# Kernel optimization log

Measured on AMD Instinct MI355X. Metric: run time of the kernel, lower is better.

## Reference

```python
import jax, jax.numpy as jnp
import numpy as np

LN_EPS = 1e-5


def _layer_norm(x, g, b):
    mu = x.mean(-1, keepdims=True)
    var = ((x - mu) ** 2).mean(-1, keepdims=True)
    return (x - mu) / jnp.sqrt(var + LN_EPS) * g + b


def _process_memory(mem, mem_W, mem_b, ln_g, ln_b):
    # deep memory MLP: Linear -> LayerNorm -> SiLU per layer (dropout = identity in eval)
    h = mem
    for i in range(mem_W.shape[0]):
        h = jax.nn.silu(_layer_norm(h @ mem_W[i] + mem_b[i], ln_g[i], ln_b[i]))
    return h


def setup_inputs() -> dict:
    key = jax.random.key(0)
    B, S, D, M, L = 32, 2048, 1024, 1024, 2
    ks = jax.random.split(key, 12)
    s = 0.02
    inp = {
        'inputs': jax.random.normal(ks[0], (B, S, D), dtype=jnp.float32),
        'memory_state': jnp.zeros((B, M), dtype=jnp.float32),
        'momentum_state': jnp.zeros((B, M), dtype=jnp.float32),
        # projections (stored [in, out], equivalent to torch Linear weight.T)
        'Wk': jax.random.normal(ks[1], (D, M)) * s, 'bk': jnp.zeros((M,)),
        'Wv': jax.random.normal(ks[2], (D, M)) * s, 'bv': jnp.zeros((M,)),
        # deep memory layers, stacked over num_layers
        'mem_W': jax.random.normal(ks[3], (L, M, M)) * s,
        'mem_b': jnp.zeros((L, M)),
        'ln_g': jnp.ones((L, M)),
        'ln_b': jnp.zeros((L, M)),
        # gates: in = D + M
        'Wf': jax.random.normal(ks[4], (D + M, M)) * s, 'bf': jnp.zeros((M,)),
        'Wm': jax.random.normal(ks[5], (D + M, M)) * s, 'bm': jnp.zeros((M,)),
        'Wu': jax.random.normal(ks[6], (D + M, M)) * s, 'bu': jnp.zeros((M,)),
        'eta': jnp.ones((1,)) * 0.9,
        'theta': jnp.ones((1,)) * 0.1,
    }
    return inp


def reference(inputs, memory_state, momentum_state, Wk, bk, Wv, bv,
              mem_W, mem_b, ln_g, ln_b, Wf, bf, Wm, bm, Wu, bu, eta, theta):
    keys = inputs @ Wk + bk      # [B,S,M]
    values = inputs @ Wv + bv    # [B,S,M]

    def assoc_loss(mem):
        mo = _process_memory(mem, mem_W, mem_b, ln_g, ln_b)      # [B,M]
        pred = jnp.einsum('bsm,bm->bs', keys, mo)                # bmm(keys, mo^T)
        diff = pred[..., None] - values                          # expand to [B,S,M]
        return 0.5 * jnp.mean(diff ** 2)

    surprise_grad = jax.grad(assoc_loss)(memory_state)           # [B,M]

    pooled = inputs.mean(axis=1)                                 # [B,D]
    gate_in = jnp.concatenate([pooled, memory_state], axis=-1)   # [B,D+M]
    forget_g = jax.nn.sigmoid(gate_in @ Wf + bf)
    update_g = jax.nn.sigmoid(gate_in @ Wu + bu)
    # momentum_gate computed in source but unused in the update
    _ = jax.nn.sigmoid(gate_in @ Wm + bm)

    new_momentum = eta * momentum_state + theta * surprise_grad
    new_memory = (1.0 - forget_g) * memory_state + update_g * new_momentum

    processed = _process_memory(new_memory, mem_W, mem_b, ln_g, ln_b)
    return processed, jax.lax.stop_gradient(new_memory)
```

## Files before the change

### kernel.cpp

```cpp
#include <hip/hip_runtime.h>
#include <math.h>

#define Bc 32
#define Sc 2048
#define Dc 1024
#define Mc 1024
#define LNEPS 1e-5f
#define SCv (1.f/67108864.f)

__device__ __forceinline__ float4 f4add(float4 a, float4 b) {
    return make_float4(a.x + b.x, a.y + b.y, a.z + b.z, a.w + b.w);
}

__device__ __forceinline__ void dreduce(float& a, float& b, float* sm) {
#pragma unroll
    for (int o = 32; o; o >>= 1) { a += __shfl_xor(a, o); b += __shfl_xor(b, o); }
    int w = threadIdx.x >> 6;
    if ((threadIdx.x & 63) == 0) { sm[w] = a; sm[4 + w] = b; }
    __syncthreads();
    a = sm[0] + sm[1] + sm[2] + sm[3];
    b = sm[4] + sm[5] + sm[6] + sm[7];
    __syncthreads();
}

__device__ __forceinline__ void wreduce(float& a, float& b) {
#pragma unroll
    for (int o = 32; o; o >>= 1) { a += __shfl_xor(a, o); b += __shfl_xor(b, o); }
}

__device__ __forceinline__ void nt_map(int t, int& n0i, int& b0i, int& ks) {
    int xcd = t & 7, rest = t >> 3;
    b0i = rest & 3;
    int q = rest >> 2;
    int s = q * 8 + xcd;
    ks = s >> 4; n0i = s & 15;
}
__device__ __forceinline__ void t_map(int t, int& dc, int& b, int& mc) {
    int xcd = t & 7, rest = t >> 3;
    b = rest & 31;
    int q = rest >> 5;
    int s = q * 8 + xcd;
    dc = s >> 3; mc = s & 7;
}

__device__ __forceinline__ void load_A128(float* Atile, const float* A, int b0, int k0) {
    for (int i = threadIdx.x; i < 1024; i += 256) {
        int r = i >> 7, c = i & 127;
        Atile[i] = A[(size_t)(b0 + r) * 1024 + k0 + c];
    }
}

__device__ __forceinline__ void nt_inner128v(const float* Atile, const float* W, int k0, int n0,
                                             float* P, int ks, int b0) {
    int lane = threadIdx.x & 63, bl = threadIdx.x >> 6;
    int n4 = lane & 15, kg = lane >> 4;
    const float* a0 = Atile + bl * 128;
    const float* a1 = Atile + (bl + 4) * 128;
    const float4* Wp = (const float4*)(W + (size_t)k0 * 1024 + n0);
    float4 acc0 = make_float4(0.f, 0.f, 0.f, 0.f);
    float4 acc1 = make_float4(0.f, 0.f, 0.f, 0.f);
#pragma unroll 8
    for (int i = 0; i < 32; ++i) {
        int k = i * 4 + kg;
        float4 w4 = Wp[(size_t)k * 256 + n4];
        float av0 = a0[k], av1 = a1[k];
        acc0.x = fmaf(av0, w4.x, acc0.x); acc0.y = fmaf(av0, w4.y, acc0.y);
        acc0.z = fmaf(av0, w4.z, acc0.z); acc0.w = fmaf(av0, w4.w, acc0.w);
        acc1.x = fmaf(av1, w4.x, acc1.x); acc1.y = fmaf(av1, w4.y, acc1.y);
        acc1.z = fmaf(av1, w4.z, acc1.z); acc1.w = fmaf(av1, w4.w, acc1.w);
    }
#pragma unroll
    for (int o = 16; o <= 32; o <<= 1) {
        acc0.x += __shfl_xor(acc0.x, o); acc0.y += __shfl_xor(acc0.y, o);
        acc0.z += __shfl_xor(acc0.z, o); acc0.w += __shfl_xor(acc0.w, o);
        acc1.x += __shfl_xor(acc1.x, o); acc1.y += __shfl_xor(acc1.y, o);
        acc1.z += __shfl_xor(acc1.z, o); acc1.w += __shfl_xor(acc1.w, o);
    }
    if (kg == 0) {
        size_t base = (size_t)ks * 32768 + n0 + 4 * n4;
        *(float4*)&P[base + (size_t)(b0 + bl) * 1024] = acc0;
        *(float4*)&P[base + (size_t)(b0 + bl + 4) * 1024] = acc1;
    }
}

__device__ __forceinline__ void t_inner(const float* Asl, const float* W,
                                        int dbase, int m0, float* outp) {
    int lane = threadIdx.x & 63, wv = threadIdx.x >> 6;
    int half = lane >> 5, m4 = lane & 31;
    float4 a4 = ((const float4*)Asl)[m4];
    int d0 = dbase + wv * 64 + half;
    float res = 0.f;
#pragma unroll 8
    for (int p = 0; p < 32; ++p) {
        int d = d0 + p * 2;
        float4 w4 = ((const float4*)(W + (size_t)d * 1024 + m0))[m4];
        float v = w4.x * a4.x + w4.y * a4.y + w4.z * a4.z + w4.w * a4.w;
#pragma unroll
        for (int o = 1; o < 32; o <<= 1) v += __shfl_xor(v, o);
        res = (m4 == p) ? v : res;
    }
    outp[wv * 64 + m4 * 2 + half] = res;
}

__global__ __launch_bounds__(256) void k_front(const float* __restrict__ Wv, const float* __restrict__ bv,
                        const float* __restrict__ mem, const float* __restrict__ W0,
                        float* __restrict__ wv_row, float* __restrict__ bvsum,
                        float* __restrict__ P1a) {
    __shared__ float shm[1032];
    int bid = blockIdx.x, tid = threadIdx.x;
    if (bid < 256) {
        float s1 = 0.f, s2 = 0.f, s3 = 0.f, s4 = 0.f;
        for (int m = tid; m < 1024; m += 256) {
            s1 += Wv[(size_t)bid * 1024 + m];
            s2 += Wv[(size_t)(bid + 256) * 1024 + m];
            s3 += Wv[(size_t)(bid + 512) * 1024 + m];
            s4 += Wv[(size_t)(bid + 768) * 1024 + m];
        }
        dreduce(s1, s2, shm + 1024);
        dreduce(s3, s4, shm + 1024);
        if (tid == 0) {
            wv_row[bid] = s1; wv_row[bid + 256] = s2;
            wv_row[bid + 512] = s3; wv_row[bid + 768] = s4;
        }
        if (bid == 0) {
            float v = 0.f, d2 = 0.f;
            for (int m = tid; m < 1024; m += 256) v += bv[m];
            dreduce(v, d2, shm + 1024);
            if (tid == 0) *bvsum = v;
        }
    } else {
        int n0i, b0i, ks;
        nt_map(bid - 256, n0i, b0i, ks);
        int n0 = n0i * 64, b0 = b0i * 8, k0 = ks * 128;
        load_A128(shm, mem, b0, k0);
        __syncthreads();
        nt_inner128v(shm, W0, k0, n0, P1a, ks, b0);
    }
}

__global__ __launch_bounds__(256) void k_gemm_ln(const float* __restrict__ P, const float* __restrict__ bias,
                          const float* __restrict__ g, const float* __restrict__ be,
                          const float* __restrict__ W1, float* __restrict__ Pout) {
    __shared__ float shm[1040];
    int tid = threadIdx.x;
    int n0i, b0i, ks;
    nt_map(blockIdx.x, n0i, b0i, ks);
    int n0 = n0i * 64, b0 = b0i * 8, k0 = ks * 128;
    float* Atile = shm; float* stats = shm + 1024;
    int wv = tid >> 6, lane = tid & 63;
    const float4* b4 = (const float4*)bias;
    for (int rr = 0; rr < 2; ++rr) {
        int r = wv + rr * 4, b = b0 + r;
        float s = 0.f, sq = 0.f;
#pragma unroll
        for (int q = 0; q < 4; ++q) {
            int m4 = lane + 64 * q;
            float4 z4 = b4[m4];
#pragma unroll
            for (int k2 = 0; k2 < 8; ++k2) {
                float4 v = ((const float4*)(P + (size_t)k2 * 32768 + (size_t)b * 1024))[m4];
                z4 = f4add(z4, v);
            }
            int c0 = 4 * m4 - k0;
            if ((unsigned)c0 < 128u) *(float4*)(Atile + r * 128 + c0) = z4;
            s += z4.x + z4.y + z4.z + z4.w;
            sq += z4.x * z4.x + z4.y * z4.y + z4.z * z4.z + z4.w * z4.w;
        }
        wreduce(s, sq);
        if (lane == 0) {
            float mean = s * (1.f / 1024.f);
            stats[r] = mean;
            stats[8 + r] = rsqrtf(sq * (1.f / 1024.f) - mean * mean + LNEPS);
        }
    }
    __syncthreads();
    for (int i = tid; i < 1024; i += 256) {
        int r = i >> 7, c = i & 127, m = k0 + c;
        float xh = (Atile[i] - stats[r]) * stats[8 + r];
        float y = fmaf(xh, g[m], be[m]);
        float sg = 1.f / (1.f + __expf(-y));
        Atile[i] = y * sg;
    }
    __syncthreads();
    nt_inner128v(Atile, W1, k0, n0, Pout, ks, b0);
}

__global__ __launch_bounds__(256) void k_wpart(const float* __restrict__ P2a, const float* __restrict__ memb1,
                        const float* __restrict__ lng1, const float* __restrict__ lnb1,
                        const float* __restrict__ bk, const float* __restrict__ Wk,
                        float* __restrict__ wpart, float* __restrict__ cbpart) {
    __shared__ float shm[136];
    int tid = threadIdx.x;
    int dc, b, mc;
    t_map(blockIdx.x, dc, b, mc);
    int m0 = mc * 128;
    float* red = shm + 128;
    float4 z4 = ((const float4*)memb1)[tid];
#pragma unroll
    for (int k2 = 0; k2 < 8; ++k2) {
        float4 v = ((const float4*)(P2a + (size_t)k2 * 32768 + (size_t)b * 1024))[tid];
        z4 = f4add(z4, v);
    }
    float s = z4.x + z4.y + z4.z + z4.w;
    float sq = z4.x * z4.x + z4.y * z4.y + z4.z * z4.z + z4.w * z4.w;
    int c0 = 4 * tid - m0;
    if ((unsigned)c0 < 128u) *(float4*)(shm + c0) = z4;
    dreduce(s, sq, red);
    float mean = s * (1.f / 1024.f);
    float rstd = rsqrtf(sq * (1.f / 1024.f) - mean * mean + LNEPS);
    if (tid < 128) {
        int m = m0 + tid;
        float xh = (shm[tid] - mean) * rstd;
        float y = fmaf(xh, lng1[m], lnb1[m]);
        float sg = 1.f / (1.f + __expf(-y));
        shm[tid] = y * sg;
    }
    __syncthreads();
    if (dc == 0) {
        float c = (tid < 128) ? bk[m0 + tid] * shm[tid] : 0.f;
        float d2 = 0.f;
        dreduce(c, d2, red);
        if (tid == 0) cbpart[mc * 32 + b] = c;
    }
    t_inner(shm, Wk, dc * 256, m0, wpart + (size_t)(mc * 32 + b) * 1024 + dc * 256);
}

__global__ __launch_bounds__(256) void k_bigpass(const float* __restrict__ X, const float* __restrict__ wpart,
                          const float* __restrict__ wv_row, const float* __restrict__ cbpart,
                          const float* __restrict__ bvsum,
                          float* __restrict__ t_part, float* __restrict__ p_part,
                          float* __restrict__ rs_part) {
    __shared__ float red[4][1024];
    __shared__ float rsum_s[4];
    int b = blockIdx.y, ch = blockIdx.x;
    int wv = threadIdx.x >> 6, lane = threadIdx.x & 63;
    float4 wreg[4], tacc[4], pacc[4];
    const float4* wp4 = (const float4*)wpart;
    const float4* wr4 = (const float4*)wv_row;
#pragma unroll
    for (int j = 0; j < 4; ++j) {
        int d4 = lane + 64 * j;
        float4 a = make_float4(0.f, 0.f, 0.f, 0.f);
#pragma unroll
        for (int mc = 0; mc < 8; ++mc) a = f4add(a, wp4[(size_t)(mc * 32 + b) * 256 + d4]);
        float4 wr = wr4[d4];
        wreg[j].x = 1024.f * a.x - wr.x;
        wreg[j].y = 1024.f * a.y - wr.y;
        wreg[j].z = 1024.f * a.z - wr.z;
        wreg[j].w = 1024.f * a.w - wr.w;
        tacc[j] = make_float4(0.f, 0.f, 0.f, 0.f);
        pacc[j] = make_float4(0.f, 0.f, 0.f, 0.f);
    }
    float cbs = 0.f;
#pragma unroll
    for (int mc = 0; mc < 8; ++mc) cbs += cbpart[mc * 32 + b];
    float cbv = 1024.f * cbs - *bvsum;
    float rloc = 0.f;
    int s0r = ch * 64 + wv * 16;
#pragma unroll 2
    for (int i = 0; i < 16; ++i) {
        const float4* xr = (const float4*)(X + ((size_t)b * Sc + s0r + i) * Dc);
        float4 x[4]; float pp = 0.f;
#pragma unroll
        for (int j = 0; j < 4; ++j) {
            x[j] = xr[lane + 64 * j];
            pp += x[j].x * wreg[j].x + x[j].y * wreg[j].y + x[j].z * wreg[j].z + x[j].w * wreg[j].w;
        }
#pragma unroll
        for (int o = 32; o; o >>= 1) pp += __shfl_xor(pp, o);
        float r = pp + cbv;
        rloc += r;
#pragma unroll
        for (int j = 0; j < 4; ++j) {
            tacc[j].x = fmaf(x[j].x, r, tacc[j].x);
            tacc[j].y = fmaf(x[j].y, r, tacc[j].y);
            tacc[j].z = fmaf(x[j].z, r, tacc[j].z);
            tacc[j].w = fmaf(x[j].w, r, tacc[j].w);
            pacc[j].x += x[j].x; pacc[j].y += x[j].y;
            pacc[j].z += x[j].z; pacc[j].w += x[j].w;
        }
    }
    float4* redv = (float4*)red[wv];
#pragma unroll
    for (int j = 0; j < 4; ++j) redv[lane + 64 * j] = tacc[j];
    if (lane == 0) rsum_s[wv] = rloc;
    __syncthreads();
    size_t pb = ((size_t)b * 32 + ch) * 1024;
    for (int j = 0; j < 4; ++j) {
        int d = threadIdx.x + 256 * j;
        t_part[pb + d] = red[0][d] + red[1][d] + red[2][d] + red[3][d];
    }
    if (threadIdx.x == 0) rs_part[b * 32 + ch] = rsum_s[0] + rsum_s[1] + rsum_s[2] + rsum_s[3];
    __syncthreads();
#pragma unroll
    for (int j = 0; j < 4; ++j) redv[lane + 64 * j] = pacc[j];
    __syncthreads();
    for (int j = 0; j < 4; ++j) {
        int d = threadIdx.x + 256 * j;
        p_part[pb + d] = red[0][d] + red[1][d] + red[2][d] + red[3][d];
    }
}

__global__ __launch_bounds__(256) void k_reduce(const float* __restrict__ t_part, const float* __restrict__ p_part,
                         const float* __restrict__ rs_part,
                         float* __restrict__ tbuf, float* __restrict__ pooled,
                         float* __restrict__ rsv) {
    int idx = blockIdx.x * 256 + threadIdx.x;
    int b = idx >> 8, d4 = idx & 255;
    const float4* tp = (const float4*)t_part + (size_t)b * 8192 + d4;
    const float4* pp = (const float4*)p_part + (size_t)b * 8192 + d4;
    float4 st = make_float4(0.f, 0.f, 0.f, 0.f);
    float4 sp = make_float4(0.f, 0.f, 0.f, 0.f);
#pragma unroll 8
    for (int ch = 0; ch < 32; ++ch) {
        st = f4add(st, tp[(size_t)ch * 256]);
        sp = f4add(sp, pp[(size_t)ch * 256]);
    }
    ((float4*)tbuf)[idx] = st;
    sp.x *= (1.f / 2048.f); sp.y *= (1.f / 2048.f);
    sp.z *= (1.f / 2048.f); sp.w *= (1.f / 2048.f);
    ((float4*)pooled)[idx] = sp;
    if (blockIdx.x == 0 && threadIdx.x < 32) {
        float s = 0.f;
        for (int ch = 0; ch < 32; ++ch) s += rs_part[threadIdx.x * 32 + ch];
        rsv[threadIdx.x] = s;
    }
}

__global__ __launch_bounds__(256) void k_gates(const float* __restrict__ tbuf, const float* __restrict__ pooled,
                        const float* __restrict__ mem,
                        const float* __restrict__ Wk, const float* __restrict__ Wf,
                        const float* __restrict__ Wu,
                        float* __restrict__ Pg, float* __restrict__ Pfp, float* __restrict__ Pup,
                        float* __restrict__ Pfm, float* __restrict__ Pum) {
    __shared__ float Atile[1024];
    int bid = blockIdx.x;
    int z = bid >> 9;
    int n0i, b0i, ks;
    nt_map(bid & 511, n0i, b0i, ks);
    int n0 = n0i * 64, b0 = b0i * 8, k0 = ks * 128;
    const float* A; const float* W; float* P;
    if (z == 0)      { A = tbuf;   W = Wk;                          P = Pg; }
    else if (z == 1) { A = pooled; W = Wf;                          P = Pfp; }
    else if (z == 2) { A = pooled; W = Wu;                          P = Pup; }
    else if (z == 3) { A = mem;    W = Wf + (size_t)1024 * 1024;    P = Pfm; }
    else             { A = mem;    W = Wu + (size_t)1024 * 1024;    P = Pum; }
    load_A128(Atile, A, b0, k0);
    __syncthreads();
    nt_inner128v(Atile, W, k0, n0, P, ks, b0);
}

__global__ __launch_bounds__(256) void k_lnbwd_gemmT(const float* __restrict__ Pz, const float* __restrict__ bias,
                              const float* __restrict__ g, const float* __restrict__ be,
                              const float* __restrict__ Pgrad, int mode,
                              const float* __restrict__ bk, const float* __restrict__ rsv,
                              const float* __restrict__ W, float* __restrict__ Pout) {
    __shared__ float shm[392];
    int tid = threadIdx.x;
    int dc, b, mc;
    t_map(blockIdx.x, dc, b, mc);
    int m0 = mc * 128;
    float* red = shm + 384;
    float rsb = mode ? rsv[b] : 0.f;
    float4 z4 = ((const float4*)bias)[tid];
#pragma unroll
    for (int k2 = 0; k2 < 8; ++k2) {
        float4 v = ((const float4*)(Pz + (size_t)k2 * 32768 + (size_t)b * 1024))[tid];
        z4 = f4add(z4, v);
    }
    float s = z4.x + z4.y + z4.z + z4.w;
    float sq = z4.x * z4.x + z4.y * z4.y + z4.z * z4.z + z4.w * z4.w;
    dreduce(s, sq, red);
    float mean = s * (1.f / 1024.f);
    float rstd = rsqrtf(sq * (1.f / 1024.f) - mean * mean + LNEPS);
    float4 g4 = make_float4(0.f, 0.f, 0.f, 0.f);
#pragma unroll
    for (int k2 = 0; k2 < 8; ++k2) {
        float4 v = ((const float4*)(Pgrad + (size_t)k2 * 32768 + (size_t)b * 1024))[tid];
        g4 = f4add(g4, v);
    }
    if (mode) {
        float4 bk4 = ((const float4*)bk)[tid];
        g4.x = SCv * (g4.x + bk4.x * rsb);
        g4.y = SCv * (g4.y + bk4.y * rsb);
        g4.z = SCv * (g4.z + bk4.z * rsb);
        g4.w = SCv * (g4.w + bk4.w * rsb);
    }
    float4 gg = ((const float4*)g)[tid], bb = ((const float4*)be)[tid];
    float sa = 0.f, sax = 0.f;
    float4 a4, xh4;
    {
        xh4.x = (z4.x - mean) * rstd;
        float y = fmaf(xh4.x, gg.x, bb.x);
        float sg2 = 1.f / (1.f + __expf(-y));
        a4.x = g4.x * (sg2 * (1.f + y * (1.f - sg2))) * gg.x;
        sa += a4.x; sax += a4.x * xh4.x;
        xh4.y = (z4.y - mean) * rstd;
        y = fmaf(xh4.y, gg.y, bb.y);
        sg2 = 1.f / (1.f + __expf(-y));
        a4.y = g4.y * (sg2 * (1.f + y * (1.f - sg2))) * gg.y;
        sa += a4.y; sax += a4.y * xh4.y;
        xh4.z = (z4.z - mean) * rstd;
        y = fmaf(xh4.z, gg.z, bb.z);
        sg2 = 1.f / (1.f + __expf(-y));
        a4.z = g4.z * (sg2 * (1.f + y * (1.f - sg2))) * gg.z;
        sa += a4.z; sax += a4.z * xh4.z;
        xh4.w = (z4.w - mean) * rstd;
        y = fmaf(xh4.w, gg.w, bb.w);
        sg2 = 1.f / (1.f + __expf(-y));
        a4.w = g4.w * (sg2 * (1.f + y * (1.f - sg2))) * gg.w;
        sa += a4.w; sax += a4.w * xh4.w;
    }
    int c0 = 4 * tid - m0;
    if ((unsigned)c0 < 128u) {
        *(float4*)(shm + c0) = a4;
        *(float4*)(shm + 128 + c0) = xh4;
    }
    dreduce(sa, sax, red);
    float ma = sa * (1.f / 1024.f), mx = sax * (1.f / 1024.f);
    if (tid < 128) shm[256 + tid] = rstd * (shm[tid] - ma - shm[128 + tid] * mx);
    __syncthreads();
    t_inner(shm + 256, W, dc * 256, m0, Pout + (size_t)(mc * 32 + b) * 1024 + dc * 256);
}

__global__ __launch_bounds__(256) void k_upd_g3(const float* __restrict__ Pfm, const float* __restrict__ Pfp,
                         const float* __restrict__ Pum, const float* __restrict__ Pup,
                         const float* __restrict__ surp,
                         const float* __restrict__ bf, const float* __restrict__ bu,
                         const float* __restrict__ mem, const float* __restrict__ mom,
                         const float* __restrict__ eta, const float* __restrict__ theta,
                         const float* __restrict__ W0, float* __restrict__ P3a,
                         float* __restrict__ out_nm) {
    __shared__ float Atile[1024];
    int tid = threadIdx.x;
    int n0i, b0i, ks;
    nt_map(blockIdx.x, n0i, b0i, ks);
    int n0 = n0i * 64, b0 = b0i * 8, k0 = ks * 128;
    float etav = eta[0], thv = theta[0];
    int r = tid >> 5, c4 = tid & 31, b = b0 + r;
    int m4 = (k0 >> 2) + c4;
    float4 zf = ((const float4*)bf)[m4];
    float4 zu = ((const float4*)bu)[m4];
    float4 sv = make_float4(0.f, 0.f, 0.f, 0.f);
#pragma unroll
    for (int k2 = 0; k2 < 8; ++k2) {
        size_t ob4 = (size_t)k2 * 8192 + (size_t)b * 256 + m4;
        zf = f4add(zf, f4add(((const float4*)Pfm)[ob4], ((const float4*)Pfp)[ob4]));
        zu = f4add(zu, f4add(((const float4*)Pum)[ob4], ((const float4*)Pup)[ob4]));
        sv = f4add(sv, ((const float4*)surp)[ob4]);
    }
    float4 me = ((const float4*)mem)[(size_t)b * 256 + m4];
    float4 mo = ((const float4*)mom)[(size_t)b * 256 + m4];
    float4 nm;
    {
        float f = 1.f / (1.f + __expf(-zf.x)), u = 1.f / (1.f + __expf(-zu.x));
        nm.x = (1.f - f) * me.x + u * (etav * mo.x + thv * sv.x);
        f = 1.f / (1.f + __expf(-zf.y)); u = 1.f / (1.f + __expf(-zu.y));
        nm.y = (1.f - f) * me.y + u * (etav * mo.y + thv * sv.y);
        f = 1.f / (1.f + __expf(-zf.z)); u = 1.f / (1.f + __expf(-zu.z));
        nm.z = (1.f - f) * me.z + u * (etav * mo.z + thv * sv.z);
        f = 1.f / (1.f + __expf(-zf.w)); u = 1.f / (1.f + __expf(-zu.w));
        nm.w = (1.f - f) * me.w + u * (etav * mo.w + thv * sv.w);
    }
    *(float4*)(Atile + r * 128 + 4 * c4) = nm;
    if (n0i == 0) ((float4*)out_nm)[(size_t)b * 256 + m4] = nm;
    __syncthreads();
    nt_inner128v(Atile, W0, k0, n0, P3a, ks, b0);
}

__global__ __launch_bounds__(256) void k_final(const float* __restrict__ P4a, const float* __restrict__ memb1,
                        const float* __restrict__ lng1, const float* __restrict__ lnb1,
                        float* __restrict__ out) {
    __shared__ float sm[8];
    int b = blockIdx.x, tid = threadIdx.x;
    float4 z4 = ((const float4*)memb1)[tid];
#pragma unroll
    for (int k2 = 0; k2 < 8; ++k2) {
        float4 v = ((const float4*)(P4a + (size_t)k2 * 32768 + (size_t)b * 1024))[tid];
        z4 = f4add(z4, v);
    }
    float s = z4.x + z4.y + z4.z + z4.w;
    float sq = z4.x * z4.x + z4.y * z4.y + z4.z * z4.z + z4.w * z4.w;
    dreduce(s, sq, sm);
    float mean = s * (1.f / 1024.f);
    float rstd = rsqrtf(sq * (1.f / 1024.f) - mean * mean + LNEPS);
    float4 gg = ((const float4*)lng1)[tid], bb = ((const float4*)lnb1)[tid];
    float4 o;
    {
        float xh = (z4.x - mean) * rstd, y = fmaf(xh, gg.x, bb.x);
        o.x = y / (1.f + __expf(-y));
        xh = (z4.y - mean) * rstd; y = fmaf(xh, gg.y, bb.y);
        o.y = y / (1.f + __expf(-y));
        xh = (z4.z - mean) * rstd; y = fmaf(xh, gg.z, bb.z);
        o.z = y / (1.f + __expf(-y));
        xh = (z4.w - mean) * rstd; y = fmaf(xh, gg.w, bb.w);
        o.w = y / (1.f + __expf(-y));
    }
    ((float4*)out)[(size_t)b * 256 + tid] = o;
}

extern "C" void kernel_launch(void* const* d_in, const int* in_sizes, int n_in,
                              void* d_out, int out_size, void* d_ws, size_t ws_size,
                              hipStream_t stream) {
    const float* X    = (const float*)d_in[0];
    const float* mem  = (const float*)d_in[1];
    const float* mom  = (const float*)d_in[2];
    const float* Wk   = (const float*)d_in[3];
    const float* bk   = (const float*)d_in[4];
    const float* Wv   = (const float*)d_in[5];
    const float* bv   = (const float*)d_in[6];
    const float* memW = (const float*)d_in[7];
    const float* memb = (const float*)d_in[8];
    const float* lng  = (const float*)d_in[9];
    const float* lnb  = (const float*)d_in[10];
    const float* Wf   = (const float*)d_in[11];
    const float* bf   = (const float*)d_in[12];
    const float* Wu   = (const float*)d_in[15];
    const float* bu   = (const float*)d_in[16];
    const float* eta  = (const float*)d_in[17];
    const float* theta= (const float*)d_in[18];
    float* out = (float*)d_out;

    const size_t BM = (size_t)Bc * Mc;
    float* ws = (float*)d_ws;
    float* P1a    = ws;
    float* P2a    = ws + 8 * BM;
    float* wpart  = ws + 16 * BM;
    float* Pg     = ws + 24 * BM;
    float* Pfp    = ws + 32 * BM;
    float* Pup    = ws + 40 * BM;
    float* Pfm    = ws + 48 * BM;
    float* Pum    = ws + 56 * BM;
    float* ghp    = ws + 64 * BM;
    float* surp   = ws + 72 * BM;
    float* P3a    = ws + 80 * BM;
    float* P4a    = ws + 88 * BM;
    float* t_part = ws + 96 * BM;
    float* p_part = ws + 128 * BM;
    float* tbuf   = ws + 160 * BM;
    float* pooled = ws + 161 * BM;
    float* wv_row = ws + 162 * BM;
    float* bvsum  = wv_row + 1024;
    float* cbpart = bvsum + 1;
    float* rs_part= cbpart + 256;
    float* rsv    = rs_part + 1024;

    const float* W0 = memW;
    const float* W1 = memW + (size_t)Mc * Mc;

    k_front<<<768, 256, 0, stream>>>(Wv, bv, mem, W0, wv_row, bvsum, P1a);
    k_gemm_ln<<<512, 256, 0, stream>>>(P1a, memb, lng, lnb, W1, P2a);
    k_wpart<<<1024, 256, 0, stream>>>(P2a, memb + 1024, lng + 1024, lnb + 1024, bk, Wk, wpart, cbpart);
    k_bigpass<<<dim3(32, 32), 256, 0, stream>>>(X, wpart, wv_row, cbpart, bvsum, t_part, p_part, rs_part);
    k_reduce<<<32, 256, 0, stream>>>(t_part, p_part, rs_part, tbuf, pooled, rsv);
    k_gates<<<2560, 256, 0, stream>>>(tbuf, pooled, mem, Wk, Wf, Wu, Pg, Pfp, Pup, Pfm, Pum);
    k_lnbwd_gemmT<<<1024, 256, 0, stream>>>(P2a, memb + 1024, lng + 1024, lnb + 1024, Pg, 1, bk, rsv, W1, ghp);
    k_lnbwd_gemmT<<<1024, 256, 0, stream>>>(P1a, memb, lng, lnb, ghp, 0, bk, rsv, W0, surp);
    k_upd_g3<<<512, 256, 0, stream>>>(Pfm, Pfp, Pum, Pup, surp, bf, bu, mem, mom, eta, theta, W0, P3a, out + BM);
    k_gemm_ln<<<512, 256, 0, stream>>>(P3a, memb, lng, lnb, W1, P4a);
    k_final<<<32, 256, 0, stream>>>(P4a, memb + 1024, lng + 1024, lnb + 1024, out);
}
```

Measured before the change: 162.6 us.

## Fuse small dependent kernels into persistent kernels with software grid barriers

```diff
diff --git a/kernel.cpp b/kernel.cpp
--- a/kernel.cpp
+++ b/kernel.cpp
@@ -7,6 +7,7 @@
 #define Mc 1024
 #define LNEPS 1e-5f
 #define SCv (1.f/67108864.f)
+#define AGENT __HIP_MEMORY_SCOPE_AGENT
 
 __device__ __forceinline__ float4 f4add(float4 a, float4 b) {
     return make_float4(a.x + b.x, a.y + b.y, a.z + b.z, a.w + b.w);
@@ -26,6 +27,24 @@
 __device__ __forceinline__ void wreduce(float& a, float& b) {
 #pragma unroll
     for (int o = 32; o; o >>= 1) { a += __shfl_xor(a, o); b += __shfl_xor(b, o); }
+}
+
+__device__ __forceinline__ void gridbar(int* cnt, int* gen, int nblk) {
+    __syncthreads();
+    if (threadIdx.x == 0) {
+        int g = __hip_atomic_load(gen, __ATOMIC_RELAXED, AGENT);
+        __threadfence();
+        int prev = __hip_atomic_fetch_add(cnt, 1, __ATOMIC_ACQ_REL, AGENT);
+        if (prev == nblk - 1) {
+            __hip_atomic_store(cnt, 0, __ATOMIC_RELAXED, AGENT);
+            __hip_atomic_fetch_add(gen, 1, __ATOMIC_RELEASE, AGENT);
+        } else {
+            while (__hip_atomic_load(gen, __ATOMIC_RELAXED, AGENT) == g)
+                __builtin_amdgcn_s_sleep(2);
+        }
+        __threadfence();
+    }
+    __syncthreads();
 }
 
 __device__ __forceinline__ void nt_map(int t, int& n0i, int& b0i, int& ks) {
@@ -102,49 +121,13 @@
     outp[wv * 64 + m4 * 2 + half] = res;
 }
 
-__global__ __launch_bounds__(256) void k_front(const float* __restrict__ Wv, const float* __restrict__ bv,
-                        const float* __restrict__ mem, const float* __restrict__ W0,
-                        float* __restrict__ wv_row, float* __restrict__ bvsum,
-                        float* __restrict__ P1a) {
-    __shared__ float shm[1032];
-    int bid = blockIdx.x, tid = threadIdx.x;
-    if (bid < 256) {
-        float s1 = 0.f, s2 = 0.f, s3 = 0.f, s4 = 0.f;
-        for (int m = tid; m < 1024; m += 256) {
-            s1 += Wv[(size_t)bid * 1024 + m];
-            s2 += Wv[(size_t)(bid + 256) * 1024 + m];
-            s3 += Wv[(size_t)(bid + 512) * 1024 + m];
-            s4 += Wv[(size_t)(bid + 768) * 1024 + m];
-        }
-        dreduce(s1, s2, shm + 1024);
-        dreduce(s3, s4, shm + 1024);
-        if (tid == 0) {
-            wv_row[bid] = s1; wv_row[bid + 256] = s2;
-            wv_row[bid + 512] = s3; wv_row[bid + 768] = s4;
-        }
-        if (bid == 0) {
-            float v = 0.f, d2 = 0.f;
-            for (int m = tid; m < 1024; m += 256) v += bv[m];
-            dreduce(v, d2, shm + 1024);
-            if (tid == 0) *bvsum = v;
-        }
-    } else {
-        int n0i, b0i, ks;
-        nt_map(bid - 256, n0i, b0i, ks);
-        int n0 = n0i * 64, b0 = b0i * 8, k0 = ks * 128;
-        load_A128(shm, mem, b0, k0);
-        __syncthreads();
-        nt_inner128v(shm, W0, k0, n0, P1a, ks, b0);
-    }
-}
-
-__global__ __launch_bounds__(256) void k_gemm_ln(const float* __restrict__ P, const float* __restrict__ bias,
-                          const float* __restrict__ g, const float* __restrict__ be,
-                          const float* __restrict__ W1, float* __restrict__ Pout) {
-    __shared__ float shm[1040];
+
+__device__ void gemm_ln_body(float* shm, const float* P, const float* bias,
+                             const float* g, const float* be,
+                             const float* W1, float* Pout, int slice) {
     int tid = threadIdx.x;
     int n0i, b0i, ks;
-    nt_map(blockIdx.x, n0i, b0i, ks);
+    nt_map(slice, n0i, b0i, ks);
     int n0 = n0i * 64, b0 = b0i * 8, k0 = ks * 128;
     float* Atile = shm; float* stats = shm + 1024;
     int wv = tid >> 6, lane = tid & 63;
@@ -185,14 +168,13 @@
     nt_inner128v(Atile, W1, k0, n0, Pout, ks, b0);
 }
 
-__global__ __launch_bounds__(256) void k_wpart(const float* __restrict__ P2a, const float* __restrict__ memb1,
-                        const float* __restrict__ lng1, const float* __restrict__ lnb1,
-                        const float* __restrict__ bk, const float* __restrict__ Wk,
-                        float* __restrict__ wpart, float* __restrict__ cbpart) {
-    __shared__ float shm[136];
+__device__ void wpart_body(float* shm, const float* P2a, const float* memb1,
+                           const float* lng1, const float* lnb1,
+                           const float* bk, const float* Wk,
+                           float* wpart, float* cbpart, int slice) {
     int tid = threadIdx.x;
     int dc, b, mc;
-    t_map(blockIdx.x, dc, b, mc);
+    t_map(slice, dc, b, mc);
     int m0 = mc * 128;
     float* red = shm + 128;
     float4 z4 = ((const float4*)memb1)[tid];
@@ -225,140 +207,14 @@
     t_inner(shm, Wk, dc * 256, m0, wpart + (size_t)(mc * 32 + b) * 1024 + dc * 256);
 }
 
-__global__ __launch_bounds__(256) void k_bigpass(const float* __restrict__ X, const float* __restrict__ wpart,
-                          const float* __restrict__ wv_row, const float* __restrict__ cbpart,
-                          const float* __restrict__ bvsum,
-                          float* __restrict__ t_part, float* __restrict__ p_part,
-                          float* __restrict__ rs_part) {
-    __shared__ float red[4][1024];
-    __shared__ float rsum_s[4];
-    int b = blockIdx.y, ch = blockIdx.x;
-    int wv = threadIdx.x >> 6, lane = threadIdx.x & 63;
-    float4 wreg[4], tacc[4], pacc[4];
-    const float4* wp4 = (const float4*)wpart;
-    const float4* wr4 = (const float4*)wv_row;
-#pragma unroll
-    for (int j = 0; j < 4; ++j) {
-        int d4 = lane + 64 * j;
-        float4 a = make_float4(0.f, 0.f, 0.f, 0.f);
-#pragma unroll
-        for (int mc = 0; mc < 8; ++mc) a = f4add(a, wp4[(size_t)(mc * 32 + b) * 256 + d4]);
-        float4 wr = wr4[d4];
-        wreg[j].x = 1024.f * a.x - wr.x;
-        wreg[j].y = 1024.f * a.y - wr.y;
-        wreg[j].z = 1024.f * a.z - wr.z;
-        wreg[j].w = 1024.f * a.w - wr.w;
-        tacc[j] = make_float4(0.f, 0.f, 0.f, 0.f);
-        pacc[j] = make_float4(0.f, 0.f, 0.f, 0.f);
-    }
-    float cbs = 0.f;
-#pragma unroll
-    for (int mc = 0; mc < 8; ++mc) cbs += cbpart[mc * 32 + b];
-    float cbv = 1024.f * cbs - *bvsum;
-    float rloc = 0.f;
-    int s0r = ch * 64 + wv * 16;
-#pragma unroll 2
-    for (int i = 0; i < 16; ++i) {
-        const float4* xr = (const float4*)(X + ((size_t)b * Sc + s0r + i) * Dc);
-        float4 x[4]; float pp = 0.f;
-#pragma unroll
-        for (int j = 0; j < 4; ++j) {
-            x[j] = xr[lane + 64 * j];
-            pp += x[j].x * wreg[j].x + x[j].y * wreg[j].y + x[j].z * wreg[j].z + x[j].w * wreg[j].w;
-        }
-#pragma unroll
-        for (int o = 32; o; o >>= 1) pp += __shfl_xor(pp, o);
-        float r = pp + cbv;
-        rloc += r;
-#pragma unroll
-        for (int j = 0; j < 4; ++j) {
-            tacc[j].x = fmaf(x[j].x, r, tacc[j].x);
-            tacc[j].y = fmaf(x[j].y, r, tacc[j].y);
-            tacc[j].z = fmaf(x[j].z, r, tacc[j].z);
-            tacc[j].w = fmaf(x[j].w, r, tacc[j].w);
-            pacc[j].x += x[j].x; pacc[j].y += x[j].y;
-            pacc[j].z += x[j].z; pacc[j].w += x[j].w;
-        }
-    }
-    float4* redv = (float4*)red[wv];
-#pragma unroll
-    for (int j = 0; j < 4; ++j) redv[lane + 64 * j] = tacc[j];
-    if (lane == 0) rsum_s[wv] = rloc;
-    __syncthreads();
-    size_t pb = ((size_t)b * 32 + ch) * 1024;
-    for (int j = 0; j < 4; ++j) {
-        int d = threadIdx.x + 256 * j;
-        t_part[pb + d] = red[0][d] + red[1][d] + red[2][d] + red[3][d];
-    }
-    if (threadIdx.x == 0) rs_part[b * 32 + ch] = rsum_s[0] + rsum_s[1] + rsum_s[2] + rsum_s[3];
-    __syncthreads();
-#pragma unroll
-    for (int j = 0; j < 4; ++j) redv[lane + 64 * j] = pacc[j];
-    __syncthreads();
-    for (int j = 0; j < 4; ++j) {
-        int d = threadIdx.x + 256 * j;
-        p_part[pb + d] = red[0][d] + red[1][d] + red[2][d] + red[3][d];
-    }
-}
-
-__global__ __launch_bounds__(256) void k_reduce(const float* __restrict__ t_part, const float* __restrict__ p_part,
-                         const float* __restrict__ rs_part,
-                         float* __restrict__ tbuf, float* __restrict__ pooled,
-                         float* __restrict__ rsv) {
-    int idx = blockIdx.x * 256 + threadIdx.x;
-    int b = idx >> 8, d4 = idx & 255;
-    const float4* tp = (const float4*)t_part + (size_t)b * 8192 + d4;
-    const float4* pp = (const float4*)p_part + (size_t)b * 8192 + d4;
-    float4 st = make_float4(0.f, 0.f, 0.f, 0.f);
-    float4 sp = make_float4(0.f, 0.f, 0.f, 0.f);
-#pragma unroll 8
-    for (int ch = 0; ch < 32; ++ch) {
-        st = f4add(st, tp[(size_t)ch * 256]);
-        sp = f4add(sp, pp[(size_t)ch * 256]);
-    }
-    ((float4*)tbuf)[idx] = st;
-    sp.x *= (1.f / 2048.f); sp.y *= (1.f / 2048.f);
-    sp.z *= (1.f / 2048.f); sp.w *= (1.f / 2048.f);
-    ((float4*)pooled)[idx] = sp;
-    if (blockIdx.x == 0 && threadIdx.x < 32) {
-        float s = 0.f;
-        for (int ch = 0; ch < 32; ++ch) s += rs_part[threadIdx.x * 32 + ch];
-        rsv[threadIdx.x] = s;
-    }
-}
-
-__global__ __launch_bounds__(256) void k_gates(const float* __restrict__ tbuf, const float* __restrict__ pooled,
-                        const float* __restrict__ mem,
-                        const float* __restrict__ Wk, const float* __restrict__ Wf,
-                        const float* __restrict__ Wu,
-                        float* __restrict__ Pg, float* __restrict__ Pfp, float* __restrict__ Pup,
-                        float* __restrict__ Pfm, float* __restrict__ Pum) {
-    __shared__ float Atile[1024];
-    int bid = blockIdx.x;
-    int z = bid >> 9;
-    int n0i, b0i, ks;
-    nt_map(bid & 511, n0i, b0i, ks);
-    int n0 = n0i * 64, b0 = b0i * 8, k0 = ks * 128;
-    const float* A; const float* W; float* P;
-    if (z == 0)      { A = tbuf;   W = Wk;                          P = Pg; }
-    else if (z == 1) { A = pooled; W = Wf;                          P = Pfp; }
-    else if (z == 2) { A = pooled; W = Wu;                          P = Pup; }
-    else if (z == 3) { A = mem;    W = Wf + (size_t)1024 * 1024;    P = Pfm; }
-    else             { A = mem;    W = Wu + (size_t)1024 * 1024;    P = Pum; }
-    load_A128(Atile, A, b0, k0);
-    __syncthreads();
-    nt_inner128v(Atile, W, k0, n0, P, ks, b0);
-}
-
-__global__ __launch_bounds__(256) void k_lnbwd_gemmT(const float* __restrict__ Pz, const float* __restrict__ bias,
-                              const float* __restrict__ g, const float* __restrict__ be,
-                              const float* __restrict__ Pgrad, int mode,
-                              const float* __restrict__ bk, const float* __restrict__ rsv,
-                              const float* __restrict__ W, float* __restrict__ Pout) {
-    __shared__ float shm[392];
+__device__ void lnbwd_body(float* shm, const float* Pz, const float* bias,
+                           const float* g, const float* be,
+                           const float* Pgrad, int mode,
+                           const float* bk, const float* rsv,
+                           const float* W, float* Pout, int slice) {
     int tid = threadIdx.x;
     int dc, b, mc;
-    t_map(blockIdx.x, dc, b, mc);
+    t_map(slice, dc, b, mc);
     int m0 = mc * 128;
     float* red = shm + 384;
     float rsb = mode ? rsv[b] : 0.f;
@@ -423,18 +279,15 @@
     t_inner(shm + 256, W, dc * 256, m0, Pout + (size_t)(mc * 32 + b) * 1024 + dc * 256);
 }
 
-__global__ __launch_bounds__(256) void k_upd_g3(const float* __restrict__ Pfm, const float* __restrict__ Pfp,
-                         const float* __restrict__ Pum, const float* __restrict__ Pup,
-                         const float* __restrict__ surp,
-                         const float* __restrict__ bf, const float* __restrict__ bu,
-                         const float* __restrict__ mem, const float* __restrict__ mom,
-                         const float* __restrict__ eta, const float* __restrict__ theta,
-                         const float* __restrict__ W0, float* __restrict__ P3a,
-                         float* __restrict__ out_nm) {
-    __shared__ float Atile[1024];
+__device__ void upd_body(float* Atile, const float* Pfm, const float* Pfp,
+                         const float* Pum, const float* Pup, const float* surp,
+                         const float* bf, const float* bu,
+                         const float* mem, const float* mom,
+                         const float* eta, const float* theta,
+                         const float* W0, float* P3a, float* out_nm, int slice) {
     int tid = threadIdx.x;
     int n0i, b0i, ks;
-    nt_map(blockIdx.x, n0i, b0i, ks);
+    nt_map(slice, n0i, b0i, ks);
     int n0 = n0i * 64, b0 = b0i * 8, k0 = ks * 128;
     float etav = eta[0], thv = theta[0];
     int r = tid >> 5, c4 = tid & 31, b = b0 + r;
@@ -468,35 +321,248 @@
     nt_inner128v(Atile, W0, k0, n0, P3a, ks, b0);
 }
 
-__global__ __launch_bounds__(256) void k_final(const float* __restrict__ P4a, const float* __restrict__ memb1,
-                        const float* __restrict__ lng1, const float* __restrict__ lnb1,
-                        float* __restrict__ out) {
-    __shared__ float sm[8];
-    int b = blockIdx.x, tid = threadIdx.x;
-    float4 z4 = ((const float4*)memb1)[tid];
-#pragma unroll
-    for (int k2 = 0; k2 < 8; ++k2) {
-        float4 v = ((const float4*)(P4a + (size_t)k2 * 32768 + (size_t)b * 1024))[tid];
-        z4 = f4add(z4, v);
-    }
-    float s = z4.x + z4.y + z4.z + z4.w;
-    float sq = z4.x * z4.x + z4.y * z4.y + z4.z * z4.z + z4.w * z4.w;
-    dreduce(s, sq, sm);
-    float mean = s * (1.f / 1024.f);
-    float rstd = rsqrtf(sq * (1.f / 1024.f) - mean * mean + LNEPS);
-    float4 gg = ((const float4*)lng1)[tid], bb = ((const float4*)lnb1)[tid];
-    float4 o;
+
+__global__ void k_init(int* bar) {
+    if (threadIdx.x < 8) bar[threadIdx.x] = 0;
+}
+
+__global__ __launch_bounds__(256, 2) void k_pre(
+        const float* __restrict__ Wv, const float* __restrict__ bv,
+        const float* __restrict__ mem, const float* __restrict__ W0,
+        const float* __restrict__ W1,
+        const float* __restrict__ memb0, const float* __restrict__ lng0, const float* __restrict__ lnb0,
+        const float* __restrict__ memb1, const float* __restrict__ lng1, const float* __restrict__ lnb1,
+        const float* __restrict__ bk, const float* __restrict__ Wk,
+        float* __restrict__ wv_row, float* __restrict__ bvsum,
+        float* __restrict__ P1a, float* __restrict__ P2a,
+        float* __restrict__ wpart, float* __restrict__ cbpart, int* bar) {
+    __shared__ float shm[1040];
+    int bid = blockIdx.x, tid = threadIdx.x;
+    for (int rr = 0; rr < 2; ++rr) {
+        int row = bid * 2 + rr;
+        float4 v4 = ((const float4*)(Wv + (size_t)row * 1024))[tid];
+        float s = v4.x + v4.y + v4.z + v4.w, d2 = 0.f;
+        dreduce(s, d2, shm + 1032);
+        if (tid == 0) wv_row[row] = s;
+    }
+    if (bid == 0) {
+        float4 v4 = ((const float4*)bv)[tid];
+        float s = v4.x + v4.y + v4.z + v4.w, d2 = 0.f;
+        dreduce(s, d2, shm + 1032);
+        if (tid == 0) *bvsum = s;
+    }
     {
-        float xh = (z4.x - mean) * rstd, y = fmaf(xh, gg.x, bb.x);
-        o.x = y / (1.f + __expf(-y));
-        xh = (z4.y - mean) * rstd; y = fmaf(xh, gg.y, bb.y);
-        o.y = y / (1.f + __expf(-y));
-        xh = (z4.z - mean) * rstd; y = fmaf(xh, gg.z, bb.z);
-        o.z = y / (1.f + __expf(-y));
-        xh = (z4.w - mean) * rstd; y = fmaf(xh, gg.w, bb.w);
-        o.w = y / (1.f + __expf(-y));
-    }
-    ((float4*)out)[(size_t)b * 256 + tid] = o;
+        int n0i, b0i, ks;
+        nt_map(bid, n0i, b0i, ks);
+        int n0 = n0i * 64, b0 = b0i * 8, k0 = ks * 128;
+        load_A128(shm, mem, b0, k0);
+        __syncthreads();
+        nt_inner128v(shm, W0, k0, n0, P1a, ks, b0);
+    }
+    gridbar(bar, bar + 1, 512);
+    gemm_ln_body(shm, P1a, memb0, lng0, lnb0, W1, P2a, bid);
+    gridbar(bar, bar + 1, 512);
+    wpart_body(shm, P2a, memb1, lng1, lnb1, bk, Wk, wpart, cbpart, bid);
+    __syncthreads();
+    wpart_body(shm, P2a, memb1, lng1, lnb1, bk, Wk, wpart, cbpart, bid + 512);
+}
+
+__global__ __launch_bounds__(256) void k_bigpass(
+        const float* __restrict__ X, const float* __restrict__ wpart,
+        const float* __restrict__ wv_row, const float* __restrict__ cbpart,
+        const float* __restrict__ bvsum, const float* __restrict__ mem,
+        const float* __restrict__ Wfb, const float* __restrict__ Wub,
+        float* __restrict__ t_part, float* __restrict__ p_part,
+        float* __restrict__ rs_part,
+        float* __restrict__ Pfm, float* __restrict__ Pum) {
+    __shared__ float red[4][1024];
+    __shared__ float rsum_s[4];
+    int bid = blockIdx.x;
+    if (bid >= 1024) {
+        int t = bid - 1024, z = t >> 9;
+        int n0i, b0i, ks;
+        nt_map(t & 511, n0i, b0i, ks);
+        int n0 = n0i * 64, b0 = b0i * 8, k0 = ks * 128;
+        float* Atile = &red[0][0];
+        load_A128(Atile, mem, b0, k0);
+        __syncthreads();
+        if (z == 0) nt_inner128v(Atile, Wfb, k0, n0, Pfm, ks, b0);
+        else        nt_inner128v(Atile, Wub, k0, n0, Pum, ks, b0);
+        return;
+    }
+    int b = bid >> 5, ch = bid & 31;
+    int wv = threadIdx.x >> 6, lane = threadIdx.x & 63;
+    float4 wreg[4], tacc[4], pacc[4];
+    const float4* wp4 = (const float4*)wpart;
+    const float4* wr4 = (const float4*)wv_row;
+#pragma unroll
+    for (int j = 0; j < 4; ++j) {
+        int d4 = lane + 64 * j;
+        float4 a = make_float4(0.f, 0.f, 0.f, 0.f);
+#pragma unroll
+        for (int mc = 0; mc < 8; ++mc) a = f4add(a, wp4[(size_t)(mc * 32 + b) * 256 + d4]);
+        float4 wr = wr4[d4];
+        wreg[j].x = 1024.f * a.x - wr.x;
+        wreg[j].y = 1024.f * a.y - wr.y;
+        wreg[j].z = 1024.f * a.z - wr.z;
+        wreg[j].w = 1024.f * a.w - wr.w;
+        tacc[j] = make_float4(0.f, 0.f, 0.f, 0.f);
+        pacc[j] = make_float4(0.f, 0.f, 0.f, 0.f);
+    }
+    float cbs = 0.f;
+#pragma unroll
+    for (int mc = 0; mc < 8; ++mc) cbs += cbpart[mc * 32 + b];
+    float cbv = 1024.f * cbs - *bvsum;
+    float rloc = 0.f;
+    int s0r = ch * 64 + wv * 16;
+#pragma unroll 2
+    for (int i = 0; i < 16; ++i) {
+        const float4* xr = (const float4*)(X + ((size_t)b * Sc + s0r + i) * Dc);
+        float4 x[4]; float pp = 0.f;
+#pragma unroll
+        for (int j = 0; j < 4; ++j) {
+            x[j] = xr[lane + 64 * j];
+            pp += x[j].x * wreg[j].x + x[j].y * wreg[j].y + x[j].z * wreg[j].z + x[j].w * wreg[j].w;
+        }
+#pragma unroll
+        for (int o = 32; o; o >>= 1) pp += __shfl_xor(pp, o);
+        float r = pp + cbv;
+        rloc += r;
+#pragma unroll
+        for (int j = 0; j < 4; ++j) {
+            tacc[j].x = fmaf(x[j].x, r, tacc[j].x);
+            tacc[j].y = fmaf(x[j].y, r, tacc[j].y);
+            tacc[j].z = fmaf(x[j].z, r, tacc[j].z);
+            tacc[j].w = fmaf(x[j].w, r, tacc[j].w);
+            pacc[j].x += x[j].x; pacc[j].y += x[j].y;
+            pacc[j].z += x[j].z; pacc[j].w += x[j].w;
+        }
+    }
+    float4* redv = (float4*)red[wv];
+#pragma unroll
+    for (int j = 0; j < 4; ++j) redv[lane + 64 * j] = tacc[j];
+    if (lane == 0) rsum_s[wv] = rloc;
+    __syncthreads();
+    size_t pb = ((size_t)b * 32 + ch) * 1024;
+    for (int j = 0; j < 4; ++j) {
+        int d = threadIdx.x + 256 * j;
+        t_part[pb + d] = red[0][d] + red[1][d] + red[2][d] + red[3][d];
+    }
+    if (threadIdx.x == 0) rs_part[b * 32 + ch] = rsum_s[0] + rsum_s[1] + rsum_s[2] + rsum_s[3];
+    __syncthreads();
+#pragma unroll
+    for (int j = 0; j < 4; ++j) redv[lane + 64 * j] = pacc[j];
+    __syncthreads();
+    for (int j = 0; j < 4; ++j) {
+        int d = threadIdx.x + 256 * j;
+        p_part[pb + d] = red[0][d] + red[1][d] + red[2][d] + red[3][d];
+    }
+}
+
+__global__ __launch_bounds__(256, 2) void k_tail(
+        const float* __restrict__ t_part, const float* __restrict__ p_part,
+        const float* __restrict__ rs_part,
+        float* __restrict__ tbuf, float* __restrict__ pooled, float* __restrict__ rsv,
+        const float* __restrict__ mem, const float* __restrict__ mom,
+        const float* __restrict__ Wk, const float* __restrict__ Wf, const float* __restrict__ Wu,
+        const float* __restrict__ W0, const float* __restrict__ W1,
+        const float* __restrict__ memb0, const float* __restrict__ lng0, const float* __restrict__ lnb0,
+        const float* __restrict__ memb1, const float* __restrict__ lng1, const float* __restrict__ lnb1,
+        const float* __restrict__ bk, const float* __restrict__ bf, const float* __restrict__ bu,
+        const float* __restrict__ eta, const float* __restrict__ theta,
+        const float* __restrict__ P1a, const float* __restrict__ P2a,
+        float* __restrict__ Pg, float* __restrict__ Pfp, float* __restrict__ Pup,
+        const float* __restrict__ Pfm, const float* __restrict__ Pum,
+        float* __restrict__ ghp, float* __restrict__ surp,
+        float* __restrict__ P3a, float* __restrict__ P4a,
+        float* __restrict__ out, int* bar) {
+    __shared__ float shm[1040];
+    int bid = blockIdx.x, tid = threadIdx.x;
+    const size_t BM = (size_t)Bc * Mc;
+    {
+        int wv = tid >> 6, lane = tid & 63;
+        int slotlocal = wv * 4 + (lane >> 4);
+        int c = lane & 15;
+        int idx = bid * 16 + slotlocal;
+        int b = idx >> 8, d4 = idx & 255;
+        const float4* tp = (const float4*)t_part + (size_t)b * 8192 + d4;
+        const float4* pp = (const float4*)p_part + (size_t)b * 8192 + d4;
+        float4 st = f4add(tp[(size_t)c * 256], tp[(size_t)(c + 16) * 256]);
+        float4 sp = f4add(pp[(size_t)c * 256], pp[(size_t)(c + 16) * 256]);
+#pragma unroll
+        for (int o = 1; o < 16; o <<= 1) {
+            st.x += __shfl_xor(st.x, o); st.y += __shfl_xor(st.y, o);
+            st.z += __shfl_xor(st.z, o); st.w += __shfl_xor(st.w, o);
+            sp.x += __shfl_xor(sp.x, o); sp.y += __shfl_xor(sp.y, o);
+            sp.z += __shfl_xor(sp.z, o); sp.w += __shfl_xor(sp.w, o);
+        }
+        if (c == 0) {
+            ((float4*)tbuf)[idx] = st;
+            sp.x *= (1.f / 2048.f); sp.y *= (1.f / 2048.f);
+            sp.z *= (1.f / 2048.f); sp.w *= (1.f / 2048.f);
+            ((float4*)pooled)[idx] = sp;
+        }
+        if (bid == 0 && tid < 32) {
+            float s = 0.f;
+            for (int ch = 0; ch < 32; ++ch) s += rs_part[tid * 32 + ch];
+            rsv[tid] = s;
+        }
+    }
+    gridbar(bar, bar + 1, 512);
+    {
+        int n0i, b0i, ks;
+        nt_map(bid, n0i, b0i, ks);
+        int n0 = n0i * 64, b0 = b0i * 8, k0 = ks * 128;
+        load_A128(shm, tbuf, b0, k0);
+        __syncthreads();
+        nt_inner128v(shm, Wk, k0, n0, Pg, ks, b0);
+        __syncthreads();
+        load_A128(shm, pooled, b0, k0);
+        __syncthreads();
+        nt_inner128v(shm, Wf, k0, n0, Pfp, ks, b0);
+        nt_inner128v(shm, Wu, k0, n0, Pup, ks, b0);
+    }
+    gridbar(bar, bar + 1, 512);
+    lnbwd_body(shm, P2a, memb1, lng1, lnb1, Pg, 1, bk, rsv, W1, ghp, bid);
+    __syncthreads();
+    lnbwd_body(shm, P2a, memb1, lng1, lnb1, Pg, 1, bk, rsv, W1, ghp, bid + 512);
+    gridbar(bar, bar + 1, 512);
+    lnbwd_body(shm, P1a, memb0, lng0, lnb0, ghp, 0, bk, rsv, W0, surp, bid);
+    __syncthreads();
+    lnbwd_body(shm, P1a, memb0, lng0, lnb0, ghp, 0, bk, rsv, W0, surp, bid + 512);
+    gridbar(bar, bar + 1, 512);
+    upd_body(shm, Pfm, Pfp, Pum, Pup, surp, bf, bu, mem, mom, eta, theta,
+             W0, P3a, out + BM, bid);
+    gridbar(bar, bar + 1, 512);
+    gemm_ln_body(shm, P3a, memb0, lng0, lnb0, W1, P4a, bid);
+    gridbar(bar, bar + 1, 512);
+    if (bid < 32) {
+        int b = bid;
+        float4 z4 = ((const float4*)memb1)[tid];
+#pragma unroll
+        for (int k2 = 0; k2 < 8; ++k2) {
+            float4 v = ((const float4*)(P4a + (size_t)k2 * 32768 + (size_t)b * 1024))[tid];
+            z4 = f4add(z4, v);
+        }
+        float s = z4.x + z4.y + z4.z + z4.w;
+        float sq = z4.x * z4.x + z4.y * z4.y + z4.z * z4.z + z4.w * z4.w;
+        dreduce(s, sq, shm);
+        float mean = s * (1.f / 1024.f);
+        float rstd = rsqrtf(sq * (1.f / 1024.f) - mean * mean + LNEPS);
+        float4 gg = ((const float4*)lng1)[tid], bb = ((const float4*)lnb1)[tid];
+        float4 o;
+        {
+            float xh = (z4.x - mean) * rstd, y = fmaf(xh, gg.x, bb.x);
+            o.x = y / (1.f + __expf(-y));
+            xh = (z4.y - mean) * rstd; y = fmaf(xh, gg.y, bb.y);
+            o.y = y / (1.f + __expf(-y));
+            xh = (z4.z - mean) * rstd; y = fmaf(xh, gg.z, bb.z);
+            o.z = y / (1.f + __expf(-y));
+            xh = (z4.w - mean) * rstd; y = fmaf(xh, gg.w, bb.w);
+            o.w = y / (1.f + __expf(-y));
+        }
+        ((float4*)out)[(size_t)b * 256 + tid] = o;
+    }
 }
 
 extern "C" void kernel_launch(void* const* d_in, const int* in_sizes, int n_in,
@@ -544,19 +610,23 @@
     float* cbpart = bvsum + 1;
     float* rs_part= cbpart + 256;
     float* rsv    = rs_part + 1024;
+    int*   bar    = (int*)(rsv + 32);
 
     const float* W0 = memW;
     const float* W1 = memW + (size_t)Mc * Mc;
-
-    k_front<<<768, 256, 0, stream>>>(Wv, bv, mem, W0, wv_row, bvsum, P1a);
-    k_gemm_ln<<<512, 256, 0, stream>>>(P1a, memb, lng, lnb, W1, P2a);
-    k_wpart<<<1024, 256, 0, stream>>>(P2a, memb + 1024, lng + 1024, lnb + 1024, bk, Wk, wpart, cbpart);
-    k_bigpass<<<dim3(32, 32), 256, 0, stream>>>(X, wpart, wv_row, cbpart, bvsum, t_part, p_part, rs_part);
-    k_reduce<<<32, 256, 0, stream>>>(t_part, p_part, rs_part, tbuf, pooled, rsv);
-    k_gates<<<2560, 256, 0, stream>>>(tbuf, pooled, mem, Wk, Wf, Wu, Pg, Pfp, Pup, Pfm, Pum);
-    k_lnbwd_gemmT<<<1024, 256, 0, stream>>>(P2a, memb + 1024, lng + 1024, lnb + 1024, Pg, 1, bk, rsv, W1, ghp);
-    k_lnbwd_gemmT<<<1024, 256, 0, stream>>>(P1a, memb, lng, lnb, ghp, 0, bk, rsv, W0, surp);
-    k_upd_g3<<<512, 256, 0, stream>>>(Pfm, Pfp, Pum, Pup, surp, bf, bu, mem, mom, eta, theta, W0, P3a, out + BM);
-    k_gemm_ln<<<512, 256, 0, stream>>>(P3a, memb, lng, lnb, W1, P4a);
-    k_final<<<32, 256, 0, stream>>>(P4a, memb + 1024, lng + 1024, lnb + 1024, out);
-}
+    const float* Wfb = Wf + (size_t)1024 * 1024;
+    const float* Wub = Wu + (size_t)1024 * 1024;
+
+    k_init<<<1, 64, 0, stream>>>(bar);
+    k_pre<<<512, 256, 0, stream>>>(Wv, bv, mem, W0, W1,
+                                   memb, lng, lnb, memb + 1024, lng + 1024, lnb + 1024,
+                                   bk, Wk, wv_row, bvsum, P1a, P2a, wpart, cbpart, bar);
+    k_bigpass<<<2048, 256, 0, stream>>>(X, wpart, wv_row, cbpart, bvsum, mem, Wfb, Wub,
+                                        t_part, p_part, rs_part, Pfm, Pum);
+    k_tail<<<512, 256, 0, stream>>>(t_part, p_part, rs_part, tbuf, pooled, rsv,
+                                    mem, mom, Wk, Wf, Wu, W0, W1,
+                                    memb, lng, lnb, memb + 1024, lng + 1024, lnb + 1024,
+                                    bk, bf, bu, eta, theta,
+                                    P1a, P2a, Pg, Pfp, Pup, Pfm, Pum,
+                                    ghp, surp, P3a, P4a, out, bar + 4);
+}
```

After: 589.3 us. 262% more time.
